# Performance work log

Measured on AMD Instinct MI355X. Metric: run time of the kernel, lower is better.

The kernel has to match this reference:

```python
import jax, jax.numpy as jnp
import numpy as np

GRID_H, GRID_W = 496, 432  # config.grid_shape
BN_EPS = 1e-5


def setup_inputs() -> dict:
    key = jax.random.key(0)
    k1, k2, k3 = jax.random.split(key, 3)
    B, D, P, N, C = 4, 4, 12000, 100, 64
    x = jax.random.normal(k1, (B, D, P, N), dtype=jnp.float32)
    indices = jax.random.randint(k2, (B, P, 2), 0, GRID_W, dtype=jnp.int32)
    W = jax.random.normal(k3, (C, D), dtype=jnp.float32) / np.sqrt(D)
    gamma = jnp.ones((C,), dtype=jnp.float32)
    beta = jnp.zeros((C,), dtype=jnp.float32)
    return {"x": x, "indices": indices, "W": W, "gamma": gamma, "beta": beta}


def reference(x, indices, W, gamma, beta):
    # 1x1 conv (bias=False): [B, D, P, N] x [C, D] -> [B, C, P, N]
    y = jnp.einsum('bdpn,cd->bcpn', x, W)
    # BatchNorm2d (training-mode batch statistics, biased variance)
    mean = jnp.mean(y, axis=(0, 2, 3), keepdims=True)
    var = jnp.var(y, axis=(0, 2, 3), keepdims=True)
    y = (y - mean) * jax.lax.rsqrt(var + BN_EPS)
    y = y * gamma.reshape(1, -1, 1, 1) + beta.reshape(1, -1, 1, 1)
    y = jax.nn.relu(y)
    # MaxPool2d((1, N)) then squeeze -> [B, C, P]
    p = jnp.max(y, axis=3)
    # scatter: per-batch index_add into flattened BEV grid
    pillars = jnp.transpose(p, (0, 2, 1))  # [B, P, C]
    flat_idx = indices[..., 0] * GRID_W + indices[..., 1]  # [B, P]
    grid = jax.vmap(
        lambda v, i: jax.ops.segment_sum(v, i, num_segments=GRID_H * GRID_W)
    )(pillars, flat_idx)  # [B, H*W, C]
    C = pillars.shape[-1]
    out = grid.reshape(-1, GRID_H, GRID_W, C)
    return jnp.transpose(out, (0, 3, 1, 2))  # [B, C, H, W]
```

## Files before the change

kernel.cpp:

```cpp
#include <hip/hip_runtime.h>

#define B_ 4
#define D_ 4
#define P_ 12000
#define N_ 100
#define C_ 64
#define GH 496
#define GW 432
#define PN (P_*N_)
#define HW (GH*GW)
#define WPB 12
#define PPB (WPB*8)
#define GRID_F (B_*(P_/PPB))
#define OVFCAP 4096
#define OCH 768
#define ONCH (HW/OCH)

typedef float v2f __attribute__((ext_vector_type(2)));

#if defined(__has_builtin)
#if __has_builtin(__builtin_elementwise_fma)
#define HAVE_EW_FMA 1
#endif
#endif
__device__ __forceinline__ v2f fma2(v2f a, v2f b, v2f c) {
#ifdef HAVE_EW_FMA
    return __builtin_elementwise_fma(a, b, c);
#else
    v2f r; r.x = fmaf(a.x, b.x, c.x); r.y = fmaf(a.y, b.y, c.y); return r;
#endif
}
__device__ __forceinline__ v2f max2(v2f a, v2f b) {
    v2f r; r.x = fmaxf(a.x, b.x); r.y = fmaxf(a.y, b.y); return r;
}

static constexpr size_t OFF_ST    = 0;
static constexpr size_t OFF_PART  = 512;
static constexpr size_t PART_BYTES= 14*(size_t)GRID_F*4;
static constexpr size_t OFF_CTL   = (OFF_PART + PART_BYTES + 63) & ~(size_t)63;
static constexpr size_t OFF_SLOT  = 28672;
static constexpr size_t SLOT_BYTES= (size_t)B_*HW*4;
static constexpr size_t OFF_OVF   = OFF_SLOT + SLOT_BYTES;
static constexpr size_t OFF_U     = OFF_OVF + (size_t)OVFCAP*4;
static constexpr size_t U_BYTES   = (size_t)B_*P_*C_*4;

template<int CTRL>
__device__ __forceinline__ float dppmax(float v) {
    int s = __builtin_amdgcn_update_dpp(0, __float_as_int(v), CTRL, 0xf, 0xf, true);
    return fmaxf(v, __int_as_float(s));
}

__global__ __launch_bounds__(256) void k_alloc(const int* __restrict__ idx,
                                               int* __restrict__ slot,
                                               int* __restrict__ ovf,
                                               int* __restrict__ ovfcnt) {
    const int BPB = (P_ + 255)/256;
    int b = blockIdx.x / BPB;
    int p = (blockIdx.x % BPB)*256 + threadIdx.x;
    if (p >= P_) return;
    size_t bp = (size_t)b*P_ + p;
    int h = idx[bp*2], w = idx[bp*2 + 1];
    int cell = h*GW + w;
    int old = atomicMax(&slot[(size_t)b*HW + cell], p);
    if (old != -1) {
        int loser = (old < p) ? old : p;
        int at = atomicAdd(ovfcnt, 1);
        if (at < OVFCAP) ovf[at] = b*P_ + loser;
    }
}

__global__ __launch_bounds__(768) void k_fused(const float* __restrict__ x,
                                               const float* __restrict__ Wm,
                                               float* __restrict__ partials,
                                               float* __restrict__ uraw) {
    __shared__ float tr[WPB][8*65 + 8];
    __shared__ float red[WPB][14];
    const int BPB = P_/PPB;
    int b    = blockIdx.x / BPB;
    int pblk = (blockIdx.x % BPB)*PPB;
    int lane = threadIdx.x & 63;
    int wv   = threadIdx.x >> 6;
    int pl   = lane >> 3;
    int oct  = lane & 7;
    int p    = pblk + wv*8 + pl;
    const float* xb = x + (size_t)b*D_*PN + (size_t)p*N_;

    float4 xq[3][4];
    #pragma unroll
    for (int j = 0; j < 3; ++j) {
        int n = 4*oct + 32*j;
        #pragma unroll
        for (int d = 0; d < 4; ++d)
            xq[j][d] = *reinterpret_cast<const float4*>(xb + n + (size_t)d*PN);
    }
    float x13[4];
    #pragma unroll
    for (int d = 0; d < 4; ++d)
        x13[d] = (oct < 4) ? xb[96 + oct + (size_t)d*PN] : xq[0][d].x;

    {
        v2f s01 = {0.f,0.f}, s23 = {0.f,0.f};
        v2f a0 = {0.f,0.f}, a1 = {0.f,0.f}, a2 = {0.f,0.f}, a3 = {0.f,0.f}, a4 = {0.f,0.f};
        #pragma unroll
        for (int j = 0; j < 3; ++j) {
            #pragma unroll
            for (int e = 0; e < 4; ++e) {
                float x0 = ((const float*)&xq[j][0])[e];
                float x1 = ((const float*)&xq[j][1])[e];
                float x2 = ((const float*)&xq[j][2])[e];
                float x3 = ((const float*)&xq[j][3])[e];
                v2f q01 = {x0,x1}, q12 = {x1,x2}, q23 = {x2,x3}, q02 = {x0,x2}, q33 = {x3,x3};
                s01 += q01; s23 += q23;
                a0 = fma2(q01, q01, a0);
                a1 = fma2(q01, q12, a1);
                a2 = fma2(q01, q23, a2);
                a3 = fma2(q02, q33, a3);
                a4 = fma2(q23, q23, a4);
            }
        }
        if (oct < 4) {
            float x0 = x13[0], x1 = x13[1], x2 = x13[2], x3 = x13[3];
            v2f q01 = {x0,x1}, q12 = {x1,x2}, q23 = {x2,x3}, q02 = {x0,x2}, q33 = {x3,x3};
            s01 += q01; s23 += q23;
            a0 = fma2(q01, q01, a0);
            a1 = fma2(q01, q12, a1);
            a2 = fma2(q01, q23, a2);
            a3 = fma2(q02, q33, a3);
            a4 = fma2(q23, q23, a4);
        }
        float v[14] = {s01.x, s01.y, s23.x, s23.y,
                       a0.x, a1.x, a2.x, a3.x,
                       a0.y, a1.y, a2.y,
                       a4.x, a3.y, a4.y};
        #pragma unroll
        for (int j = 0; j < 14; ++j) {
            float t = v[j];
            #pragma unroll
            for (int off = 32; off; off >>= 1) t += __shfl_down(t, off);
            if (lane == 0) red[wv][j] = t;
        }
        __syncthreads();
        if (threadIdx.x < 14) {
            int j = threadIdx.x;
            float t = 0.f;
            #pragma unroll
            for (int w2 = 0; w2 < WPB; ++w2) t += red[w2][j];
            partials[(size_t)j*GRID_F + blockIdx.x] = t;
        }
    }

    for (int c = 0; c < C_; c += 2) {
        const float4 wA = *reinterpret_cast<const float4*>(Wm + c*4);
        const float4 wB = *reinterpret_cast<const float4*>(Wm + (c+1)*4);
        v2f wp0 = {wA.x, wB.x}, wp1 = {wA.y, wB.y};
        v2f wp2 = {wA.z, wB.z}, wp3 = {wA.w, wB.w};
        v2f m = {-3.4e38f, -3.4e38f};
        #pragma unroll
        for (int j = 0; j < 3; ++j) {
            #pragma unroll
            for (int e = 0; e < 4; ++e) {
                float v0 = ((const float*)&xq[j][0])[e];
                float v1 = ((const float*)&xq[j][1])[e];
                float v2 = ((const float*)&xq[j][2])[e];
                float v3 = ((const float*)&xq[j][3])[e];
                v2f dot = wp3 * v3;
                dot = fma2(wp2, v2f{v2, v2}, dot);
                dot = fma2(wp1, v2f{v1, v1}, dot);
                dot = fma2(wp0, v2f{v0, v0}, dot);
                m = max2(m, dot);
            }
        }
        {
            v2f dot = wp3 * x13[3];
            dot = fma2(wp2, v2f{x13[2], x13[2]}, dot);
            dot = fma2(wp1, v2f{x13[1], x13[1]}, dot);
            dot = fma2(wp0, v2f{x13[0], x13[0]}, dot);
            m = max2(m, dot);
        }
        float mA = m.x, mB = m.y;
        mA = dppmax<0xB1>(mA); mA = dppmax<0x4E>(mA); mA = dppmax<0x141>(mA);
        mB = dppmax<0xB1>(mB); mB = dppmax<0x4E>(mB); mB = dppmax<0x141>(mB);
        if (oct == (c >> 3)) {
            tr[wv][pl*65 + c]     = mA;
            tr[wv][pl*65 + c + 1] = mB;
        }
    }
    __builtin_amdgcn_s_waitcnt(0);
    for (int pi = 0; pi < 8; ++pi)
        uraw[((size_t)b*P_ + pblk + wv*8 + pi)*C_ + lane] = tr[wv][pi*65 + lane];
}

__global__ __launch_bounds__(256) void k_stats(const float* __restrict__ partials,
                                               const float* __restrict__ Wm,
                                               const float* __restrict__ gamma,
                                               const float* __restrict__ beta,
                                               float* __restrict__ st) {
    __shared__ double mom_s[14];
    __shared__ double redd[4];
    int lane = threadIdx.x & 63, wv = threadIdx.x >> 6;
    for (int j = 0; j < 14; ++j) {
        double s = 0.0;
        for (int i = threadIdx.x; i < GRID_F; i += 256)
            s += (double)partials[(size_t)j*GRID_F + i];
        #pragma unroll
        for (int off = 32; off; off >>= 1) s += __shfl_down(s, off);
        if (lane == 0) redd[wv] = s;
        __syncthreads();
        if (threadIdx.x == 0) mom_s[j] = redd[0]+redd[1]+redd[2]+redd[3];
        __syncthreads();
    }
    if (threadIdx.x < C_) {
        int c = threadIdx.x;
        double S[4];
        #pragma unroll
        for (int d = 0; d < 4; ++d) S[d] = mom_s[d];
        double M[4][4];
        int k = 4;
        for (int i = 0; i < 4; ++i)
            for (int j = i; j < 4; ++j) { M[i][j] = mom_s[k]; M[j][i] = mom_s[k]; ++k; }
        double w[4];
        #pragma unroll
        for (int d = 0; d < 4; ++d) w[d] = (double)Wm[c*4+d];
        const double NT = (double)B_ * (double)PN;
        double mean = 0.0;
        #pragma unroll
        for (int d = 0; d < 4; ++d) mean += w[d]*S[d];
        mean /= NT;
        double ey2 = 0.0;
        for (int i = 0; i < 4; ++i)
            for (int j = 0; j < 4; ++j) ey2 += w[i]*w[j]*M[i][j];
        ey2 /= NT;
        double var = ey2 - mean*mean;
        double inv = 1.0 / sqrt(var + 1e-5);
        double sc  = (double)gamma[c] * inv;
        st[c*2]     = (float)sc;
        st[c*2 + 1] = (float)((double)beta[c] - mean*sc);
    }
}

__global__ __launch_bounds__(256) void k_out(const int* __restrict__ slot,
                                             const float* __restrict__ uraw,
                                             const float* __restrict__ st,
                                             float* __restrict__ out) {
    __shared__ float tile[8][OCH];
    __shared__ int   sslot[OCH];
    int b     = blockIdx.x / ONCH;
    int chunk = blockIdx.x % ONCH;
    int cell0 = chunk*OCH;
    int t = threadIdx.x;
    #pragma unroll
    for (int k = 0; k < OCH/256; ++k)
        sslot[k*256 + t] = slot[(size_t)b*HW + cell0 + k*256 + t];
    __syncthreads();
    const float* vb = uraw + (size_t)b*P_*C_;
    for (int g = 0; g < 8; ++g) {
        #pragma unroll
        for (int k = 0; k < OCH/256; ++k) {
            int cell = k*256 + t;
            int s = sslot[cell];
            float4 u0 = {0.f,0.f,0.f,0.f}, u1 = {0.f,0.f,0.f,0.f};
            if (s >= 0) {
                const float* up = vb + (size_t)s*C_ + g*8;
                u0 = *reinterpret_cast<const float4*>(up);
                u1 = *reinterpret_cast<const float4*>(up + 4);
            }
            tile[0][cell] = u0.x; tile[1][cell] = u0.y;
            tile[2][cell] = u0.z; tile[3][cell] = u0.w;
            tile[4][cell] = u1.x; tile[5][cell] = u1.y;
            tile[6][cell] = u1.z; tile[7][cell] = u1.w;
        }
        __syncthreads();
        #pragma unroll
        for (int cp = 0; cp < 8; ++cp) {
            int c = g*8 + cp;
            float2 ss = *reinterpret_cast<const float2*>(st + c*2);
            float* ob = out + ((size_t)b*C_ + c)*HW + cell0;
            #pragma unroll
            for (int k = 0; k < OCH/256; ++k) {
                int cell = k*256 + t;
                float y = 0.f;
                if (sslot[cell] >= 0)
                    y = fmaxf(fmaf(ss.x, tile[cp][cell], ss.y), 0.f);
                ob[cell] = y;
            }
        }
        __syncthreads();
    }
}

__global__ __launch_bounds__(256) void k_fixup(const int* __restrict__ ovf,
                                               const int* __restrict__ ovfcnt,
                                               const int* __restrict__ idx,
                                               const float* __restrict__ uraw,
                                               const float* __restrict__ st,
                                               float* __restrict__ out) {
    int n = *ovfcnt;
    if (n > OVFCAP) n = OVFCAP;
    int lane = threadIdx.x & 63;
    int wid  = (blockIdx.x*256 + threadIdx.x) >> 6;
    int nw   = gridDim.x*4;
    float2 ss = *reinterpret_cast<const float2*>(st + lane*2);
    for (int e = wid; e < n; e += nw) {
        int bp = ovf[e];
        int b  = bp / P_;
        int h = idx[(size_t)bp*2], w = idx[(size_t)bp*2 + 1];
        int cell = h*GW + w;
        float u = uraw[(size_t)bp*C_ + lane];
        float y = fmaxf(fmaf(ss.x, u, ss.y), 0.0f);
        if (y > 0.0f)
            atomicAdd(&out[((size_t)b*C_ + lane)*HW + cell], y);
    }
}

extern "C" void kernel_launch(void* const* d_in, const int* in_sizes, int n_in,
                              void* d_out, int out_size, void* d_ws, size_t ws_size,
                              hipStream_t stream) {
    const float* x     = (const float*)d_in[0];
    const int*   idx   = (const int*)  d_in[1];
    const float* Wm    = (const float*)d_in[2];
    const float* gamma = (const float*)d_in[3];
    const float* beta  = (const float*)d_in[4];
    float* out = (float*)d_out;

    char* ws = (char*)d_ws;
    float* st       = (float*)(ws + OFF_ST);
    float* partials = (float*)(ws + OFF_PART);
    int*   ovfcnt   = (int*)  (ws + OFF_CTL);
    int*   slot     = (int*)  (ws + OFF_SLOT);
    int*   ovf      = (int*)  (ws + OFF_OVF);
    float* uraw     = (float*)(ws + OFF_U);

    hipMemsetAsync(ws + OFF_SLOT, 0xFF, SLOT_BYTES, stream);
    hipMemsetAsync(ws + OFF_CTL, 0, 64, stream);
    k_alloc<<<B_*((P_ + 255)/256), 256, 0, stream>>>(idx, slot, ovf, ovfcnt);
    k_fused<<<GRID_F, WPB*64, 0, stream>>>(x, Wm, partials, uraw);
    k_stats<<<1, 256, 0, stream>>>(partials, Wm, gamma, beta, st);
    k_out  <<<B_*ONCH, 256, 0, stream>>>(slot, uraw, st, out);
    k_fixup<<<32, 256, 0, stream>>>(ovf, ovfcnt, idx, uraw, st, out);
}
```

Baseline: 150.0 us.

## Fold BN stats into output kernels and store pooled pillar features in fp16

Drops the single-block k_stats launch. Every k_out and k_fixup block now recomputes the 14 moment sums and the per-channel scale and shift itself, into shared memory. The pooled per-pillar values are also stored as fp16 instead of fp32, which halves the intermediate buffer's write and gather traffic. The cost is redundant reduction work in every block (about a thousand blocks each re-reading the partials array) and a loss of precision in the pre-normalization values.

Result: no change. 151.5 us (+1.0%).

```diff
diff --git a/kernel.cpp b/kernel.cpp
--- a/kernel.cpp
+++ b/kernel.cpp
@@ -1,4 +1,5 @@
 #include <hip/hip_runtime.h>
+#include <hip/hip_fp16.h>
 
 #define B_ 4
 #define D_ 4
@@ -34,20 +35,65 @@
     v2f r; r.x = fmaxf(a.x, b.x); r.y = fmaxf(a.y, b.y); return r;
 }
 
-static constexpr size_t OFF_ST    = 0;
-static constexpr size_t OFF_PART  = 512;
+static constexpr size_t OFF_PART  = 0;
 static constexpr size_t PART_BYTES= 14*(size_t)GRID_F*4;
 static constexpr size_t OFF_CTL   = (OFF_PART + PART_BYTES + 63) & ~(size_t)63;
 static constexpr size_t OFF_SLOT  = 28672;
 static constexpr size_t SLOT_BYTES= (size_t)B_*HW*4;
 static constexpr size_t OFF_OVF   = OFF_SLOT + SLOT_BYTES;
 static constexpr size_t OFF_U     = OFF_OVF + (size_t)OVFCAP*4;
-static constexpr size_t U_BYTES   = (size_t)B_*P_*C_*4;
+static constexpr size_t U_BYTES   = (size_t)B_*P_*C_*2;
 
 template<int CTRL>
 __device__ __forceinline__ float dppmax(float v) {
     int s = __builtin_amdgcn_update_dpp(0, __float_as_int(v), CTRL, 0xf, 0xf, true);
     return fmaxf(v, __int_as_float(s));
+}
+
+__device__ __forceinline__ void block_stats(const float* __restrict__ partials,
+                                            const float* __restrict__ Wm,
+                                            const float* __restrict__ gamma,
+                                            const float* __restrict__ beta,
+                                            double* smom ,
+                                            float*  sst  ) {
+    int t = threadIdx.x;
+    if (t < 224) {
+        int j = t >> 4, l = t & 15;
+        double s = 0.0;
+        for (int i = l; i < GRID_F; i += 16)
+            s += (double)partials[(size_t)j*GRID_F + i];
+        #pragma unroll
+        for (int off = 8; off; off >>= 1) s += __shfl_down(s, off);
+        if (l == 0) smom[j] = s;
+    }
+    __syncthreads();
+    if (t < C_) {
+        int c = t;
+        double S[4];
+        #pragma unroll
+        for (int d = 0; d < 4; ++d) S[d] = smom[d];
+        double M[4][4];
+        int k = 4;
+        for (int i = 0; i < 4; ++i)
+            for (int j = i; j < 4; ++j) { M[i][j] = smom[k]; M[j][i] = smom[k]; ++k; }
+        double w[4];
+        #pragma unroll
+        for (int d = 0; d < 4; ++d) w[d] = (double)Wm[c*4+d];
+        const double NT = (double)B_ * (double)PN;
+        double mean = 0.0;
+        #pragma unroll
+        for (int d = 0; d < 4; ++d) mean += w[d]*S[d];
+        mean /= NT;
+        double ey2 = 0.0;
+        for (int i = 0; i < 4; ++i)
+            for (int j = 0; j < 4; ++j) ey2 += w[i]*w[j]*M[i][j];
+        ey2 /= NT;
+        double var = ey2 - mean*mean;
+        double inv = 1.0 / sqrt(var + 1e-5);
+        double sc  = (double)gamma[c] * inv;
+        sst[c*2]     = (float)sc;
+        sst[c*2 + 1] = (float)((double)beta[c] - mean*sc);
+    }
 }
 
 __global__ __launch_bounds__(256) void k_alloc(const int* __restrict__ idx,
@@ -72,7 +118,7 @@
 __global__ __launch_bounds__(768) void k_fused(const float* __restrict__ x,
                                                const float* __restrict__ Wm,
                                                float* __restrict__ partials,
-                                               float* __restrict__ uraw) {
+                                               __half* __restrict__ uraw) {
     __shared__ float tr[WPB][8*65 + 8];
     __shared__ float red[WPB][14];
     const int BPB = P_/PPB;
@@ -187,100 +233,60 @@
     }
     __builtin_amdgcn_s_waitcnt(0);
     for (int pi = 0; pi < 8; ++pi)
-        uraw[((size_t)b*P_ + pblk + wv*8 + pi)*C_ + lane] = tr[wv][pi*65 + lane];
-}
-
-__global__ __launch_bounds__(256) void k_stats(const float* __restrict__ partials,
-                                               const float* __restrict__ Wm,
-                                               const float* __restrict__ gamma,
-                                               const float* __restrict__ beta,
-                                               float* __restrict__ st) {
-    __shared__ double mom_s[14];
-    __shared__ double redd[4];
-    int lane = threadIdx.x & 63, wv = threadIdx.x >> 6;
-    for (int j = 0; j < 14; ++j) {
-        double s = 0.0;
-        for (int i = threadIdx.x; i < GRID_F; i += 256)
-            s += (double)partials[(size_t)j*GRID_F + i];
-        #pragma unroll
-        for (int off = 32; off; off >>= 1) s += __shfl_down(s, off);
-        if (lane == 0) redd[wv] = s;
-        __syncthreads();
-        if (threadIdx.x == 0) mom_s[j] = redd[0]+redd[1]+redd[2]+redd[3];
-        __syncthreads();
-    }
-    if (threadIdx.x < C_) {
-        int c = threadIdx.x;
-        double S[4];
-        #pragma unroll
-        for (int d = 0; d < 4; ++d) S[d] = mom_s[d];
-        double M[4][4];
-        int k = 4;
-        for (int i = 0; i < 4; ++i)
-            for (int j = i; j < 4; ++j) { M[i][j] = mom_s[k]; M[j][i] = mom_s[k]; ++k; }
-        double w[4];
-        #pragma unroll
-        for (int d = 0; d < 4; ++d) w[d] = (double)Wm[c*4+d];
-        const double NT = (double)B_ * (double)PN;
-        double mean = 0.0;
-        #pragma unroll
-        for (int d = 0; d < 4; ++d) mean += w[d]*S[d];
-        mean /= NT;
-        double ey2 = 0.0;
-        for (int i = 0; i < 4; ++i)
-            for (int j = 0; j < 4; ++j) ey2 += w[i]*w[j]*M[i][j];
-        ey2 /= NT;
-        double var = ey2 - mean*mean;
-        double inv = 1.0 / sqrt(var + 1e-5);
-        double sc  = (double)gamma[c] * inv;
-        st[c*2]     = (float)sc;
-        st[c*2 + 1] = (float)((double)beta[c] - mean*sc);
-    }
+        uraw[((size_t)b*P_ + pblk + wv*8 + pi)*C_ + lane] =
+            __float2half(tr[wv][pi*65 + lane]);
 }
 
 __global__ __launch_bounds__(256) void k_out(const int* __restrict__ slot,
-                                             const float* __restrict__ uraw,
-                                             const float* __restrict__ st,
+                                             const __half* __restrict__ uraw,
+                                             const float* __restrict__ partials,
+                                             const float* __restrict__ Wm,
+                                             const float* __restrict__ gamma,
+                                             const float* __restrict__ beta,
                                              float* __restrict__ out) {
     __shared__ float tile[8][OCH];
     __shared__ int   sslot[OCH];
+    __shared__ double smom[14];
+    __shared__ float  sst[128];
     int b     = blockIdx.x / ONCH;
     int chunk = blockIdx.x % ONCH;
     int cell0 = chunk*OCH;
     int t = threadIdx.x;
+    block_stats(partials, Wm, gamma, beta, smom, sst);
     #pragma unroll
     for (int k = 0; k < OCH/256; ++k)
         sslot[k*256 + t] = slot[(size_t)b*HW + cell0 + k*256 + t];
     __syncthreads();
-    const float* vb = uraw + (size_t)b*P_*C_;
+    const __half* vb = uraw + (size_t)b*P_*C_;
     for (int g = 0; g < 8; ++g) {
         #pragma unroll
         for (int k = 0; k < OCH/256; ++k) {
             int cell = k*256 + t;
             int s = sslot[cell];
-            float4 u0 = {0.f,0.f,0.f,0.f}, u1 = {0.f,0.f,0.f,0.f};
             if (s >= 0) {
-                const float* up = vb + (size_t)s*C_ + g*8;
-                u0 = *reinterpret_cast<const float4*>(up);
-                u1 = *reinterpret_cast<const float4*>(up + 4);
+                float4 raw = *reinterpret_cast<const float4*>(vb + (size_t)s*C_ + g*8);
+                const __half2* h2 = reinterpret_cast<const __half2*>(&raw);
+                tile[0][cell] = __low2float(h2[0]); tile[1][cell] = __high2float(h2[0]);
+                tile[2][cell] = __low2float(h2[1]); tile[3][cell] = __high2float(h2[1]);
+                tile[4][cell] = __low2float(h2[2]); tile[5][cell] = __high2float(h2[2]);
+                tile[6][cell] = __low2float(h2[3]); tile[7][cell] = __high2float(h2[3]);
+            } else {
+                #pragma unroll
+                for (int q = 0; q < 8; ++q) tile[q][cell] = 0.f;
             }
-            tile[0][cell] = u0.x; tile[1][cell] = u0.y;
-            tile[2][cell] = u0.z; tile[3][cell] = u0.w;
-            tile[4][cell] = u1.x; tile[5][cell] = u1.y;
-            tile[6][cell] = u1.z; tile[7][cell] = u1.w;
         }
         __syncthreads();
         #pragma unroll
         for (int cp = 0; cp < 8; ++cp) {
             int c = g*8 + cp;
-            float2 ss = *reinterpret_cast<const float2*>(st + c*2);
+            float scc = sst[c*2], shc = sst[c*2+1];
             float* ob = out + ((size_t)b*C_ + c)*HW + cell0;
             #pragma unroll
             for (int k = 0; k < OCH/256; ++k) {
                 int cell = k*256 + t;
                 float y = 0.f;
                 if (sslot[cell] >= 0)
-                    y = fmaxf(fmaf(ss.x, tile[cp][cell], ss.y), 0.f);
+                    y = fmaxf(fmaf(scc, tile[cp][cell], shc), 0.f);
                 ob[cell] = y;
             }
         }
@@ -291,22 +297,29 @@
 __global__ __launch_bounds__(256) void k_fixup(const int* __restrict__ ovf,
                                                const int* __restrict__ ovfcnt,
                                                const int* __restrict__ idx,
-                                               const float* __restrict__ uraw,
-                                               const float* __restrict__ st,
+                                               const __half* __restrict__ uraw,
+                                               const float* __restrict__ partials,
+                                               const float* __restrict__ Wm,
+                                               const float* __restrict__ gamma,
+                                               const float* __restrict__ beta,
                                                float* __restrict__ out) {
+    __shared__ double smom[14];
+    __shared__ float  sst[128];
+    block_stats(partials, Wm, gamma, beta, smom, sst);
+    __syncthreads();
     int n = *ovfcnt;
     if (n > OVFCAP) n = OVFCAP;
     int lane = threadIdx.x & 63;
     int wid  = (blockIdx.x*256 + threadIdx.x) >> 6;
     int nw   = gridDim.x*4;
-    float2 ss = *reinterpret_cast<const float2*>(st + lane*2);
+    float scc = sst[lane*2], shc = sst[lane*2+1];
     for (int e = wid; e < n; e += nw) {
         int bp = ovf[e];
         int b  = bp / P_;
         int h = idx[(size_t)bp*2], w = idx[(size_t)bp*2 + 1];
         int cell = h*GW + w;
-        float u = uraw[(size_t)bp*C_ + lane];
-        float y = fmaxf(fmaf(ss.x, u, ss.y), 0.0f);
+        float u = __half2float(uraw[(size_t)bp*C_ + lane]);
+        float y = fmaxf(fmaf(scc, u, shc), 0.0f);
         if (y > 0.0f)
             atomicAdd(&out[((size_t)b*C_ + lane)*HW + cell], y);
     }
@@ -323,18 +336,16 @@
     float* out = (float*)d_out;
 
     char* ws = (char*)d_ws;
-    float* st       = (float*)(ws + OFF_ST);
-    float* partials = (float*)(ws + OFF_PART);
-    int*   ovfcnt   = (int*)  (ws + OFF_CTL);
-    int*   slot     = (int*)  (ws + OFF_SLOT);
-    int*   ovf      = (int*)  (ws + OFF_OVF);
-    float* uraw     = (float*)(ws + OFF_U);
+    float*  partials = (float*) (ws + OFF_PART);
+    int*    ovfcnt   = (int*)   (ws + OFF_CTL);
+    int*    slot     = (int*)   (ws + OFF_SLOT);
+    int*    ovf      = (int*)   (ws + OFF_OVF);
+    __half* uraw     = (__half*)(ws + OFF_U);
 
     hipMemsetAsync(ws + OFF_SLOT, 0xFF, SLOT_BYTES, stream);
     hipMemsetAsync(ws + OFF_CTL, 0, 64, stream);
     k_alloc<<<B_*((P_ + 255)/256), 256, 0, stream>>>(idx, slot, ovf, ovfcnt);
     k_fused<<<GRID_F, WPB*64, 0, stream>>>(x, Wm, partials, uraw);
-    k_stats<<<1, 256, 0, stream>>>(partials, Wm, gamma, beta, st);
-    k_out  <<<B_*ONCH, 256, 0, stream>>>(slot, uraw, st, out);
-    k_fixup<<<32, 256, 0, stream>>>(ovf, ovfcnt, idx, uraw, st, out);
-}
+    k_out  <<<B_*ONCH, 256, 0, stream>>>(slot, uraw, partials, Wm, gamma, beta, out);
+    k_fixup<<<32, 256, 0, stream>>>(ovf, ovfcnt, idx, uraw, partials, Wm, gamma, beta, out);
+}
```
